# Performance work log

Hardware: AMD Instinct MI355X
Metric: run time of the kernel (lower is better)

The kernel has to match this reference:

```python
import jax, jax.numpy as jnp
import numpy as np
import math

D_MODEL = 1024
N_HEADS = 16
HEAD_DIM = D_MODEL // N_HEADS
B, T = 4, 2048


def setup_inputs() -> dict:
    key = jax.random.key(0)
    k1, k2, k3, k4, k5 = jax.random.split(key, 5)
    s = 1.0 / math.sqrt(D_MODEL)
    return {
        "x": jax.random.normal(k1, (B, T, D_MODEL), dtype=jnp.float32),
        "qkv_w": jax.random.normal(k2, (3 * D_MODEL, D_MODEL), dtype=jnp.float32) * s,
        "qkv_b": jax.random.normal(k3, (3 * D_MODEL,), dtype=jnp.float32) * 0.02,
        "out_w": jax.random.normal(k4, (D_MODEL, D_MODEL), dtype=jnp.float32) * s,
        "out_b": jax.random.normal(k5, (D_MODEL,), dtype=jnp.float32) * 0.02,
    }


def reference(x, qkv_w, qkv_b, out_w, out_b) -> jnp.ndarray:
    b, t, c = x.shape
    h, hd = N_HEADS, HEAD_DIM
    # qkv projection: [B,T,3C]
    qkv = jnp.einsum("btc,oc->bto", x, qkv_w) + qkv_b
    qkv = qkv.reshape(b, t, 3, h, hd).transpose(2, 0, 3, 1, 4)  # [3,B,H,T,hd]
    q, k, v = qkv[0], qkv[1], qkv[2]
    scale = 1.0 / math.sqrt(hd)
    attn = jnp.einsum("bhqd,bhkd->bhqk", q, k) * scale  # [B,H,T,T]
    causal = jnp.triu(jnp.ones((t, t), dtype=bool), k=1)
    attn = jnp.where(causal, -jnp.inf, attn)
    attn = jax.nn.softmax(attn, axis=-1)
    out = jnp.einsum("bhqk,bhkd->bhqd", attn, v)  # [B,H,T,hd]
    out = out.transpose(0, 2, 1, 3).reshape(b, t, c)
    return jnp.einsum("btc,oc->bto", out, out_w) + out_b
```

## Files before the change

kernel.cpp:

```cpp
#include <hip/hip_runtime.h>
#include <stdint.h>
#include <stddef.h>

#define TT 2048
#define NH 16
#define HD 64
#define CM 1024
#define QSCALE 0.1803368801f
#define PPAD 72

typedef float f32x4  __attribute__((ext_vector_type(4)));
typedef short bf16x8 __attribute__((ext_vector_type(8)));

static __device__ __forceinline__ unsigned short f32_to_bf16(float f) {
    union { float f; unsigned u; } c; c.f = f;
    unsigned u = c.u;
    u += 0x7FFFu + ((u >> 16) & 1u);
    return (unsigned short)(u >> 16);
}

static __device__ __forceinline__ unsigned pack_bf16_trunc(float lo, float hi) {
    return __builtin_amdgcn_perm(__float_as_uint(hi), __float_as_uint(lo), 0x07060302u);
}

static __device__ __forceinline__ void glds16(const unsigned short* g, unsigned short* l) {
    __builtin_amdgcn_global_load_lds(
        (const __attribute__((address_space(1))) unsigned int*)g,
        (__attribute__((address_space(3))) unsigned int*)l,
        16, 0, 0);
}

static __device__ __forceinline__ void hard_barrier() {
    asm volatile("s_waitcnt vmcnt(0) lgkmcnt(0)" ::: "memory");
    __syncthreads();
}

__global__ __launch_bounds__(256) void cast_all(
    const float* __restrict__ x, const float* __restrict__ w1,
    const float* __restrict__ w2,
    unsigned short* __restrict__ X16, unsigned short* __restrict__ W1o,
    unsigned short* __restrict__ W2o) {
    int i = blockIdx.x * blockDim.x + threadIdx.x;
    const float* src; unsigned short* dst; int j;
    if (i < 2097152)      { src = x;  dst = X16; j = i; }
    else if (i < 2883584) { src = w1; dst = W1o; j = i - 2097152; }
    else                  { src = w2; dst = W2o; j = i - 2883584; }
    float4 v = ((const float4*)src)[j];
    ushort4 o;
    o.x = f32_to_bf16(v.x); o.y = f32_to_bf16(v.y);
    o.z = f32_to_bf16(v.z); o.w = f32_to_bf16(v.w);
    ((ushort4*)dst)[j] = o;
}

template<bool SWAP>
__device__ __forceinline__ void gemm_core_dbuf(
    const unsigned short* __restrict__ A,
    const unsigned short* __restrict__ Bm,
    int K, int m0, int n0,
    unsigned short* lds,
    f32x4 acc[4][4])
{
    const int tid  = threadIdx.x;
    const int lane = tid & 63;
    const int wm   = ((tid >> 6) >> 1) * 64;
    const int wn   = ((tid >> 6) & 1) * 64;
    const int l15  = lane & 15;
    const int quad = lane >> 4;

    unsigned short* ldsA = lds;
    unsigned short* ldsB = lds + 8192;

    const int c1 = tid, c2 = tid + 256;
    const unsigned short* gA1 = A  + (size_t)(m0 + (c1 >> 2)) * K + (c1 & 3) * 8;
    const unsigned short* gA2 = A  + (size_t)(m0 + (c2 >> 2)) * K + (c2 & 3) * 8;
    const unsigned short* gB1 = Bm + (size_t)(n0 + (c1 >> 2)) * K + (c1 & 3) * 8;
    const unsigned short* gB2 = Bm + (size_t)(n0 + (c2 >> 2)) * K + (c2 & 3) * 8;
    unsigned short* dA1 = ldsA + (c1 & ~63) * 8;
    unsigned short* dA2 = ldsA + (c2 & ~63) * 8;
    unsigned short* dB1 = ldsB + (c1 & ~63) * 8;
    unsigned short* dB2 = ldsB + (c2 & ~63) * 8;

    glds16(gA1, dA1); glds16(gA2, dA2);
    glds16(gB1, dB1); glds16(gB2, dB2);
    gA1 += 32; gA2 += 32; gB1 += 32; gB2 += 32;

    int step = 0;
    for (int k0 = 0; k0 < K; k0 += 32, step ^= 1) {
        hard_barrier();
        if (k0 + 32 < K) {
            const int nx = (step ^ 1) * 4096;
            glds16(gA1, dA1 + nx); glds16(gA2, dA2 + nx);
            glds16(gB1, dB1 + nx); glds16(gB2, dB2 + nx);
            gA1 += 32; gA2 += 32; gB1 += 32; gB2 += 32;
        }
        const unsigned short* tA = ldsA + step * 4096;
        const unsigned short* tB = ldsB + step * 4096;

        bf16x8 af[4], bfr[4];
        #pragma unroll
        for (int mi = 0; mi < 4; ++mi)
            af[mi] = *(const bf16x8*)(tA + (wm + mi * 16 + l15) * 32 + quad * 8);
        #pragma unroll
        for (int ni = 0; ni < 4; ++ni)
            bfr[ni] = *(const bf16x8*)(tB + (wn + ni * 16 + l15) * 32 + quad * 8);

        #pragma unroll
        for (int mi = 0; mi < 4; ++mi)
            #pragma unroll
            for (int ni = 0; ni < 4; ++ni)
                acc[mi][ni] = SWAP
                    ? __builtin_amdgcn_mfma_f32_16x16x32_bf16(bfr[ni], af[mi], acc[mi][ni], 0, 0, 0)
                    : __builtin_amdgcn_mfma_f32_16x16x32_bf16(af[mi], bfr[ni], acc[mi][ni], 0, 0, 0);
    }
}

__global__ __launch_bounds__(256, 2) void gemm_qkv(
    const unsigned short* __restrict__ X,
    const unsigned short* __restrict__ W,
    const float* __restrict__ bias,
    unsigned short* __restrict__ Qb,
    unsigned short* __restrict__ Kb,
    unsigned short* __restrict__ Vt)
{
    __shared__ __align__(16) unsigned short lds[16384];
    const int m0 = blockIdx.y * 128;
    const int n0 = blockIdx.x * 128;

    f32x4 acc[4][4];
    f32x4 z = {0.f, 0.f, 0.f, 0.f};
    #pragma unroll
    for (int mi = 0; mi < 4; ++mi)
        #pragma unroll
        for (int ni = 0; ni < 4; ++ni) acc[mi][ni] = z;

    const bool qk = (n0 < 2048);
    if (qk) gemm_core_dbuf<true >(X, W, CM, m0, n0, lds, acc);
    else    gemm_core_dbuf<false>(X, W, CM, m0, n0, lds, acc);

    const int tid  = threadIdx.x;
    const int lane = tid & 63;
    const int w    = tid >> 6;
    const int wm   = (w >> 1) * 64;
    const int wn   = (w & 1) * 64;
    const int l15  = lane & 15;
    const int quad = lane >> 4;
    const int b_idx = m0 >> 11;
    const int t0 = m0 & 2047;

    if (!qk) {
        hard_barrier();
        #pragma unroll
        for (int half = 0; half < 2; ++half) {
            if ((w & 1) == half) {
                #pragma unroll
                for (int ni = 0; ni < 4; ++ni) {
                    const int orow = ni * 16 + l15;
                    const float bv = bias[n0 + half * 64 + orow];
                    #pragma unroll
                    for (int mi = 0; mi < 4; ++mi) {
                        uint2 pk;
                        pk.x = (unsigned)f32_to_bf16(acc[mi][ni][0] + bv) |
                               ((unsigned)f32_to_bf16(acc[mi][ni][1] + bv) << 16);
                        pk.y = (unsigned)f32_to_bf16(acc[mi][ni][2] + bv) |
                               ((unsigned)f32_to_bf16(acc[mi][ni][3] + bv) << 16);
                        *(uint2*)(lds + orow * 136 + wm + mi * 16 + quad * 4) = pk;
                    }
                }
            }
            hard_barrier();
            {
                const int row = tid >> 2, seg = tid & 3;
                const int o   = n0 + half * 64 + row;
                const int oin = o & 1023;
                const int hh  = oin >> 6, d = oin & 63;
                unsigned short* dst = Vt + ((size_t)((b_idx << 4) + hh) * HD + d) * TT
                                        + t0 + seg * 32;
                const unsigned short* src = lds + row * 136 + seg * 32;
                #pragma unroll
                for (int u = 0; u < 4; ++u)
                    *(uint4*)(dst + u * 8) = *(const uint4*)(src + u * 8);
            }
            hard_barrier();
        }
        return;
    }

    const int region = n0 >> 10;
    unsigned short* dst0 = region ? Kb : Qb;
    const float scl = region ? 1.0f : QSCALE;
    #pragma unroll
    for (int mi = 0; mi < 4; ++mi) {
        const int gm = m0 + wm + mi * 16 + l15;
        const int b  = gm >> 11, t = gm & 2047;
        #pragma unroll
        for (int ni = 0; ni < 4; ++ni) {
            const int o  = n0 + wn + ni * 16 + quad * 4;
            const float4 bv = *(const float4*)(bias + o);
            const int oin = o & 1023;
            const int hh = oin >> 6, d = oin & 63;
            const int bh = (b << 4) + hh;
            const float v0 = (acc[mi][ni][0] + bv.x) * scl;
            const float v1 = (acc[mi][ni][1] + bv.y) * scl;
            const float v2 = (acc[mi][ni][2] + bv.z) * scl;
            const float v3 = (acc[mi][ni][3] + bv.w) * scl;
            uint2 pk;
            pk.x = (unsigned)f32_to_bf16(v0) | ((unsigned)f32_to_bf16(v1) << 16);
            pk.y = (unsigned)f32_to_bf16(v2) | ((unsigned)f32_to_bf16(v3) << 16);
            *(uint2*)(dst0 + (((size_t)(bh * TT + t)) << 6) + d) = pk;
        }
    }
}

__global__ __launch_bounds__(256, 2) void attn_kernel(
    const unsigned short* __restrict__ Qb,
    const unsigned short* __restrict__ Kb,
    const unsigned short* __restrict__ Vt,
    unsigned short* __restrict__ CTX)
{
    __shared__ __align__(16) unsigned short Kl[2][64 * 64];
    __shared__ __align__(16) unsigned short Vl[2][64 * 64];
    __shared__ __align__(16) unsigned short Pl[8][16 * PPAD];

    const int pair = blockIdx.x;
    const int h = blockIdx.y, b = blockIdx.z;
    const int tid  = threadIdx.x;
    const int lane = tid & 63;
    const int w    = tid >> 6;
    const int l15  = lane & 15;
    const int quad = lane >> 4;
    const int sw   = l15 & 7;
    const int bh   = b * NH + h;

    const unsigned short* Kbase = Kb + (size_t)bh * TT * HD;
    const unsigned short* Vbase = Vt + (size_t)bh * HD * TT;
    const f32x4 z = {0.f, 0.f, 0.f, 0.f};

    const int c1 = tid, c2 = tid + 256;
    const int row1 = c1 >> 3, col1 = ((c1 & 7) ^ (row1 & 7)) * 8;
    const int row2 = c2 >> 3, col2 = ((c2 & 7) ^ (row2 & 7)) * 8;
    unsigned short* dK1 = &Kl[0][(c1 & ~63) * 8];
    unsigned short* dK2 = &Kl[0][(c2 & ~63) * 8];
    unsigned short* dV1 = &Vl[0][(c1 & ~63) * 8];
    unsigned short* dV2 = &Vl[0][(c2 & ~63) * 8];

    for (int j = 0; j < 2; ++j) {
        const int qt = j ? pair : 15 - pair;
        const int kt_last = 2 * qt + 1;
        const int qb0 = qt * 128;

        const unsigned short* kp1 = Kbase + (size_t)row1 * HD + col1;
        const unsigned short* kp2 = Kbase + (size_t)row2 * HD + col2;
        const unsigned short* vp1 = Vbase + (size_t)row1 * TT + col1;
        const unsigned short* vp2 = Vbase + (size_t)row2 * TT + col2;

        bf16x8 qf[2][2];
        #pragma unroll
        for (int f = 0; f < 2; ++f) {
            const unsigned short* qr =
                Qb + (size_t)(bh * TT + qb0 + f * 64 + w * 16 + l15) * HD + quad * 8;
            qf[f][0] = *(const bf16x8*)(qr);
            qf[f][1] = *(const bf16x8*)(qr + 32);
        }

        f32x4 o_acc[2][4];
        #pragma unroll
        for (int f = 0; f < 2; ++f)
            #pragma unroll
            for (int di = 0; di < 4; ++di) o_acc[f][di] = z;
        float lrun[2] = {0.f, 0.f};

        hard_barrier();
        glds16(kp1, dK1); glds16(kp2, dK2);
        glds16(vp1, dV1); glds16(vp2, dV2);
        kp1 += 64 * HD; kp2 += 64 * HD; vp1 += 64; vp2 += 64;

        for (int kt = 0; kt <= kt_last; ++kt) {
            const int cur = kt & 1;
            hard_barrier();
            if (kt < kt_last) {
                const int nx = (cur ^ 1) * 4096;
                glds16(kp1, dK1 + nx); glds16(kp2, dK2 + nx);
                glds16(vp1, dV1 + nx); glds16(vp2, dV2 + nx);
                kp1 += 64 * HD; kp2 += 64 * HD; vp1 += 64; vp2 += 64;
            }

            const unsigned short* Kt = Kl[cur];
            const unsigned short* Vtile = Vl[cur];
            const bool f0act = (kt < kt_last);

            f32x4 s0[4], s1[4];
            #pragma unroll
            for (int ni = 0; ni < 4; ++ni) {
                const unsigned short* kr = Kt + (ni * 16 + l15) * 64;
                bf16x8 kf0 = *(const bf16x8*)(kr + ((quad ^ sw) * 8));
                bf16x8 kf1 = *(const bf16x8*)(kr + (((quad + 4) ^ sw) * 8));
                if (f0act) {
                    f32x4 a = __builtin_amdgcn_mfma_f32_16x16x32_bf16(kf0, qf[0][0], z, 0, 0, 0);
                    s0[ni] = __builtin_amdgcn_mfma_f32_16x16x32_bf16(kf1, qf[0][1], a, 0, 0, 0);
                }
                f32x4 a1 = __builtin_amdgcn_mfma_f32_16x16x32_bf16(kf0, qf[1][0], z, 0, 0, 0);
                s1[ni] = __builtin_amdgcn_mfma_f32_16x16x32_bf16(kf1, qf[1][1], a1, 0, 0, 0);
            }

            const int qloc = w * 16 + l15;
            if (f0act && kt == 2 * qt) {
                #pragma unroll
                for (int ni = 0; ni < 4; ++ni)
                    #pragma unroll
                    for (int r = 0; r < 4; ++r)
                        if (ni * 16 + quad * 4 + r > qloc) s0[ni][r] = -1e30f;
            }
            if (kt == kt_last) {
                #pragma unroll
                for (int ni = 0; ni < 4; ++ni)
                    #pragma unroll
                    for (int r = 0; r < 4; ++r)
                        if (ni * 16 + quad * 4 + r > qloc) s1[ni][r] = -1e30f;
            }

            #define SOFTMAX_P(S, F)                                              \
            {                                                                    \
                float acc_l = 0.f;                                               \
                _Pragma("unroll")                                                \
                for (int ni = 0; ni < 4; ++ni)                                   \
                    _Pragma("unroll")                                            \
                    for (int r = 0; r < 4; ++r) {                                \
                        float p = __builtin_amdgcn_exp2f(S[ni][r]);              \
                        S[ni][r] = p;                                            \
                        acc_l += p;                                              \
                    }                                                            \
                lrun[F] += acc_l;                                                \
                unsigned short* pwf = Pl[w * 2 + F];                             \
                _Pragma("unroll")                                                \
                for (int ni = 0; ni < 4; ++ni) {                                 \
                    uint2 pk;                                                    \
                    pk.x = pack_bf16_trunc(S[ni][0], S[ni][1]);                  \
                    pk.y = pack_bf16_trunc(S[ni][2], S[ni][3]);                  \
                    *(uint2*)(pwf + l15 * PPAD + ni * 16 + quad * 4) = pk;       \
                }                                                                \
            }

            if (f0act) SOFTMAX_P(s0, 0);
            SOFTMAX_P(s1, 1);
            #undef SOFTMAX_P

            asm volatile("s_waitcnt lgkmcnt(0)" ::: "memory");

            const unsigned short* pw0 = Pl[w * 2 + 0];
            const unsigned short* pw1 = Pl[w * 2 + 1];
            if (f0act) {
                #pragma unroll
                for (int c = 0; c < 2; ++c) {
                    bf16x8 pf0 = *(const bf16x8*)(pw0 + l15 * PPAD + c * 32 + quad * 8);
                    bf16x8 pf1 = *(const bf16x8*)(pw1 + l15 * PPAD + c * 32 + quad * 8);
                    #pragma unroll
                    for (int di = 0; di < 4; ++di) {
                        const unsigned short* vr = Vtile + (di * 16 + l15) * 64
                                                 + (((c * 4 + quad) ^ sw) * 8);
                        bf16x8 vf = *(const bf16x8*)(vr);
                        o_acc[0][di] = __builtin_amdgcn_mfma_f32_16x16x32_bf16(vf, pf0, o_acc[0][di], 0, 0, 0);
                        o_acc[1][di] = __builtin_amdgcn_mfma_f32_16x16x32_bf16(vf, pf1, o_acc[1][di], 0, 0, 0);
                    }
                }
            } else {
                #pragma unroll
                for (int c = 0; c < 2; ++c) {
                    bf16x8 pf1 = *(const bf16x8*)(pw1 + l15 * PPAD + c * 32 + quad * 8);
                    #pragma unroll
                    for (int di = 0; di < 4; ++di) {
                        const unsigned short* vr = Vtile + (di * 16 + l15) * 64
                                                 + (((c * 4 + quad) ^ sw) * 8);
                        bf16x8 vf = *(const bf16x8*)(vr);
                        o_acc[1][di] = __builtin_amdgcn_mfma_f32_16x16x32_bf16(vf, pf1, o_acc[1][di], 0, 0, 0);
                    }
                }
            }
        }

        #pragma unroll
        for (int f = 0; f < 2; ++f) {
            float lt = lrun[f];
            lt += __shfl_xor(lt, 16);
            lt += __shfl_xor(lt, 32);
            const float inv = 1.0f / lt;
            unsigned short* crow =
                CTX + (size_t)(b * TT + qb0 + f * 64 + w * 16 + l15) * CM + h * HD;
            #pragma unroll
            for (int di = 0; di < 4; ++di) {
                uint2 pk;
                pk.x = (unsigned)f32_to_bf16(o_acc[f][di][0] * inv) |
                       ((unsigned)f32_to_bf16(o_acc[f][di][1] * inv) << 16);
                pk.y = (unsigned)f32_to_bf16(o_acc[f][di][2] * inv) |
                       ((unsigned)f32_to_bf16(o_acc[f][di][3] * inv) << 16);
                *(uint2*)(crow + di * 16 + quad * 4) = pk;
            }
        }
    }
}

__global__ __launch_bounds__(256, 2) void gemm_out(
    const unsigned short* __restrict__ CTX,
    const unsigned short* __restrict__ W,
    const float* __restrict__ bias,
    float* __restrict__ out)
{
    __shared__ __align__(16) unsigned short lds[16384];
    const int m0 = blockIdx.y * 128;
    const int n0 = blockIdx.x * 128;

    f32x4 acc[4][4];
    f32x4 z = {0.f, 0.f, 0.f, 0.f};
    #pragma unroll
    for (int mi = 0; mi < 4; ++mi)
        #pragma unroll
        for (int ni = 0; ni < 4; ++ni) acc[mi][ni] = z;

    gemm_core_dbuf<true>(CTX, W, CM, m0, n0, lds, acc);

    const int tid  = threadIdx.x;
    const int lane = tid & 63;
    const int w    = tid >> 6;
    const int wm   = (w >> 1) * 64;
    const int wn   = (w & 1) * 64;
    const int l15  = lane & 15;
    const int quad = lane >> 4;

    #pragma unroll
    for (int mi = 0; mi < 4; ++mi) {
        const int gm = m0 + wm + mi * 16 + l15;
        float* orow = out + (size_t)gm * CM;
        #pragma unroll
        for (int ni = 0; ni < 4; ++ni) {
            const int o = n0 + wn + ni * 16 + quad * 4;
            const float4 bv = *(const float4*)(bias + o);
            float4 v;
            v.x = acc[mi][ni][0] + bv.x;
            v.y = acc[mi][ni][1] + bv.y;
            v.z = acc[mi][ni][2] + bv.z;
            v.w = acc[mi][ni][3] + bv.w;
            *(float4*)(orow + o) = v;
        }
    }
}

extern "C" void kernel_launch(void* const* d_in, const int* in_sizes, int n_in,
                              void* d_out, int out_size, void* d_ws, size_t ws_size,
                              hipStream_t stream) {
    const float* x     = (const float*)d_in[0];
    const float* qkv_w = (const float*)d_in[1];
    const float* qkv_b = (const float*)d_in[2];
    const float* out_w = (const float*)d_in[3];
    const float* out_b = (const float*)d_in[4];
    float* out = (float*)d_out;

    char* ws = (char*)d_ws;
    unsigned short* X16 = (unsigned short*)(ws + 0);
    unsigned short* W1  = (unsigned short*)(ws + 16777216);
    unsigned short* W2  = (unsigned short*)(ws + 23068672);
    unsigned short* Qb  = (unsigned short*)(ws + 25165824);
    unsigned short* Kb  = (unsigned short*)(ws + 41943040);
    unsigned short* Vt  = (unsigned short*)(ws + 58720256);
    unsigned short* CTX = (unsigned short*)(ws + 75497472);

    cast_all<<<12288, 256, 0, stream>>>(x, qkv_w, out_w, X16, W1, W2);

    gemm_qkv<<<dim3(24, 64), 256, 0, stream>>>(X16, W1, qkv_b, Qb, Kb, Vt);
    attn_kernel<<<dim3(8, NH, 4), 256, 0, stream>>>(Qb, Kb, Vt, CTX);
    gemm_out<<<dim3(8, 64), 256, 0, stream>>>(CTX, W2, out_b, out);
}
```

Baseline: 262.5 us.

## Swizzle GEMM LDS layout and split attention into one q-tile per block

New measurement: 255.4 us. 1.03x faster.

```diff
diff --git a/kernel.cpp b/kernel.cpp
--- a/kernel.cpp
+++ b/kernel.cpp
@@ -66,15 +66,18 @@
     const int wn   = ((tid >> 6) & 1) * 64;
     const int l15  = lane & 15;
     const int quad = lane >> 4;
+    const int rsw  = l15 & 3;
 
     unsigned short* ldsA = lds;
     unsigned short* ldsB = lds + 8192;
 
     const int c1 = tid, c2 = tid + 256;
-    const unsigned short* gA1 = A  + (size_t)(m0 + (c1 >> 2)) * K + (c1 & 3) * 8;
-    const unsigned short* gA2 = A  + (size_t)(m0 + (c2 >> 2)) * K + (c2 & 3) * 8;
-    const unsigned short* gB1 = Bm + (size_t)(n0 + (c1 >> 2)) * K + (c1 & 3) * 8;
-    const unsigned short* gB2 = Bm + (size_t)(n0 + (c2 >> 2)) * K + (c2 & 3) * 8;
+    const int r1 = c1 >> 2, s1 = ((c1 & 3) ^ (r1 & 3)) * 8;
+    const int r2 = c2 >> 2, s2 = ((c2 & 3) ^ (r2 & 3)) * 8;
+    const unsigned short* gA1 = A  + (size_t)(m0 + r1) * K + s1;
+    const unsigned short* gA2 = A  + (size_t)(m0 + r2) * K + s2;
+    const unsigned short* gB1 = Bm + (size_t)(n0 + r1) * K + s1;
+    const unsigned short* gB2 = Bm + (size_t)(n0 + r2) * K + s2;
     unsigned short* dA1 = ldsA + (c1 & ~63) * 8;
     unsigned short* dA2 = ldsA + (c2 & ~63) * 8;
     unsigned short* dB1 = ldsB + (c1 & ~63) * 8;
@@ -95,14 +98,15 @@
         }
         const unsigned short* tA = ldsA + step * 4096;
         const unsigned short* tB = ldsB + step * 4096;
+        const int ro = (quad ^ rsw) * 8;
 
         bf16x8 af[4], bfr[4];
         #pragma unroll
         for (int mi = 0; mi < 4; ++mi)
-            af[mi] = *(const bf16x8*)(tA + (wm + mi * 16 + l15) * 32 + quad * 8);
+            af[mi] = *(const bf16x8*)(tA + (wm + mi * 16 + l15) * 32 + ro);
         #pragma unroll
         for (int ni = 0; ni < 4; ++ni)
-            bfr[ni] = *(const bf16x8*)(tB + (wn + ni * 16 + l15) * 32 + quad * 8);
+            bfr[ni] = *(const bf16x8*)(tB + (wn + ni * 16 + l15) * 32 + ro);
 
         #pragma unroll
         for (int mi = 0; mi < 4; ++mi)
@@ -221,18 +225,20 @@
     __shared__ __align__(16) unsigned short Vl[2][64 * 64];
     __shared__ __align__(16) unsigned short Pl[8][16 * PPAD];
 
-    const int pair = blockIdx.x;
-    const int h = blockIdx.y, b = blockIdx.z;
+    const int id = blockIdx.x;
+    const int qt = 15 - (id >> 6);
+    const int bh = id & 63;
+    const int b  = bh >> 4, h = bh & 15;
     const int tid  = threadIdx.x;
     const int lane = tid & 63;
     const int w    = tid >> 6;
     const int l15  = lane & 15;
     const int quad = lane >> 4;
     const int sw   = l15 & 7;
-    const int bh   = b * NH + h;
-
-    const unsigned short* Kbase = Kb + (size_t)bh * TT * HD;
-    const unsigned short* Vbase = Vt + (size_t)bh * HD * TT;
+    const int bhh  = b * NH + h;
+
+    const unsigned short* Kbase = Kb + (size_t)bhh * TT * HD;
+    const unsigned short* Vbase = Vt + (size_t)bhh * HD * TT;
     const f32x4 z = {0.f, 0.f, 0.f, 0.f};
 
     const int c1 = tid, c2 = tid + 256;
@@ -243,157 +249,153 @@
     unsigned short* dV1 = &Vl[0][(c1 & ~63) * 8];
     unsigned short* dV2 = &Vl[0][(c2 & ~63) * 8];
 
-    for (int j = 0; j < 2; ++j) {
-        const int qt = j ? pair : 15 - pair;
-        const int kt_last = 2 * qt + 1;
-        const int qb0 = qt * 128;
-
-        const unsigned short* kp1 = Kbase + (size_t)row1 * HD + col1;
-        const unsigned short* kp2 = Kbase + (size_t)row2 * HD + col2;
-        const unsigned short* vp1 = Vbase + (size_t)row1 * TT + col1;
-        const unsigned short* vp2 = Vbase + (size_t)row2 * TT + col2;
-
-        bf16x8 qf[2][2];
-        #pragma unroll
-        for (int f = 0; f < 2; ++f) {
-            const unsigned short* qr =
-                Qb + (size_t)(bh * TT + qb0 + f * 64 + w * 16 + l15) * HD + quad * 8;
-            qf[f][0] = *(const bf16x8*)(qr);
-            qf[f][1] = *(const bf16x8*)(qr + 32);
-        }
-
-        f32x4 o_acc[2][4];
-        #pragma unroll
-        for (int f = 0; f < 2; ++f)
+    const int kt_last = 2 * qt + 1;
+    const int qb0 = qt * 128;
+
+    const unsigned short* kp1 = Kbase + (size_t)row1 * HD + col1;
+    const unsigned short* kp2 = Kbase + (size_t)row2 * HD + col2;
+    const unsigned short* vp1 = Vbase + (size_t)row1 * TT + col1;
+    const unsigned short* vp2 = Vbase + (size_t)row2 * TT + col2;
+
+    bf16x8 qf[2][2];
+    #pragma unroll
+    for (int f = 0; f < 2; ++f) {
+        const unsigned short* qr =
+            Qb + (size_t)(bhh * TT + qb0 + f * 64 + w * 16 + l15) * HD + quad * 8;
+        qf[f][0] = *(const bf16x8*)(qr);
+        qf[f][1] = *(const bf16x8*)(qr + 32);
+    }
+
+    f32x4 o_acc[2][4];
+    #pragma unroll
+    for (int f = 0; f < 2; ++f)
+        #pragma unroll
+        for (int di = 0; di < 4; ++di) o_acc[f][di] = z;
+    float lrun[2] = {0.f, 0.f};
+
+    glds16(kp1, dK1); glds16(kp2, dK2);
+    glds16(vp1, dV1); glds16(vp2, dV2);
+    kp1 += 64 * HD; kp2 += 64 * HD; vp1 += 64; vp2 += 64;
+
+    for (int kt = 0; kt <= kt_last; ++kt) {
+        const int cur = kt & 1;
+        hard_barrier();
+        if (kt < kt_last) {
+            const int nx = (cur ^ 1) * 4096;
+            glds16(kp1, dK1 + nx); glds16(kp2, dK2 + nx);
+            glds16(vp1, dV1 + nx); glds16(vp2, dV2 + nx);
+            kp1 += 64 * HD; kp2 += 64 * HD; vp1 += 64; vp2 += 64;
+        }
+
+        const unsigned short* Kt = Kl[cur];
+        const unsigned short* Vtile = Vl[cur];
+        const bool f0act = (kt < kt_last);
+
+        f32x4 s0[4], s1[4];
+        #pragma unroll
+        for (int ni = 0; ni < 4; ++ni) {
+            const unsigned short* kr = Kt + (ni * 16 + l15) * 64;
+            bf16x8 kf0 = *(const bf16x8*)(kr + ((quad ^ sw) * 8));
+            bf16x8 kf1 = *(const bf16x8*)(kr + (((quad + 4) ^ sw) * 8));
+            if (f0act) {
+                f32x4 a = __builtin_amdgcn_mfma_f32_16x16x32_bf16(kf0, qf[0][0], z, 0, 0, 0);
+                s0[ni] = __builtin_amdgcn_mfma_f32_16x16x32_bf16(kf1, qf[0][1], a, 0, 0, 0);
+            }
+            f32x4 a1 = __builtin_amdgcn_mfma_f32_16x16x32_bf16(kf0, qf[1][0], z, 0, 0, 0);
+            s1[ni] = __builtin_amdgcn_mfma_f32_16x16x32_bf16(kf1, qf[1][1], a1, 0, 0, 0);
+        }
+
+        const int qloc = w * 16 + l15;
+        if (f0act && kt == 2 * qt) {
             #pragma unroll
-            for (int di = 0; di < 4; ++di) o_acc[f][di] = z;
-        float lrun[2] = {0.f, 0.f};
-
-        hard_barrier();
-        glds16(kp1, dK1); glds16(kp2, dK2);
-        glds16(vp1, dV1); glds16(vp2, dV2);
-        kp1 += 64 * HD; kp2 += 64 * HD; vp1 += 64; vp2 += 64;
-
-        for (int kt = 0; kt <= kt_last; ++kt) {
-            const int cur = kt & 1;
-            hard_barrier();
-            if (kt < kt_last) {
-                const int nx = (cur ^ 1) * 4096;
-                glds16(kp1, dK1 + nx); glds16(kp2, dK2 + nx);
-                glds16(vp1, dV1 + nx); glds16(vp2, dV2 + nx);
-                kp1 += 64 * HD; kp2 += 64 * HD; vp1 += 64; vp2 += 64;
-            }
-
-            const unsigned short* Kt = Kl[cur];
-            const unsigned short* Vtile = Vl[cur];
-            const bool f0act = (kt < kt_last);
-
-            f32x4 s0[4], s1[4];
+            for (int ni = 0; ni < 4; ++ni)
+                #pragma unroll
+                for (int r = 0; r < 4; ++r)
+                    if (ni * 16 + quad * 4 + r > qloc) s0[ni][r] = -1e30f;
+        }
+        if (kt == kt_last) {
             #pragma unroll
-            for (int ni = 0; ni < 4; ++ni) {
-                const unsigned short* kr = Kt + (ni * 16 + l15) * 64;
-                bf16x8 kf0 = *(const bf16x8*)(kr + ((quad ^ sw) * 8));
-                bf16x8 kf1 = *(const bf16x8*)(kr + (((quad + 4) ^ sw) * 8));
-                if (f0act) {
-                    f32x4 a = __builtin_amdgcn_mfma_f32_16x16x32_bf16(kf0, qf[0][0], z, 0, 0, 0);
-                    s0[ni] = __builtin_amdgcn_mfma_f32_16x16x32_bf16(kf1, qf[0][1], a, 0, 0, 0);
-                }
-                f32x4 a1 = __builtin_amdgcn_mfma_f32_16x16x32_bf16(kf0, qf[1][0], z, 0, 0, 0);
-                s1[ni] = __builtin_amdgcn_mfma_f32_16x16x32_bf16(kf1, qf[1][1], a1, 0, 0, 0);
-            }
-
-            const int qloc = w * 16 + l15;
-            if (f0act && kt == 2 * qt) {
-                #pragma unroll
-                for (int ni = 0; ni < 4; ++ni)
-                    #pragma unroll
-                    for (int r = 0; r < 4; ++r)
-                        if (ni * 16 + quad * 4 + r > qloc) s0[ni][r] = -1e30f;
-            }
-            if (kt == kt_last) {
-                #pragma unroll
-                for (int ni = 0; ni < 4; ++ni)
-                    #pragma unroll
-                    for (int r = 0; r < 4; ++r)
-                        if (ni * 16 + quad * 4 + r > qloc) s1[ni][r] = -1e30f;
-            }
-
-            #define SOFTMAX_P(S, F)                                              \
-            {                                                                    \
-                float acc_l = 0.f;                                               \
-                _Pragma("unroll")                                                \
-                for (int ni = 0; ni < 4; ++ni)                                   \
-                    _Pragma("unroll")                                            \
-                    for (int r = 0; r < 4; ++r) {                                \
-                        float p = __builtin_amdgcn_exp2f(S[ni][r]);              \
-                        S[ni][r] = p;                                            \
-                        acc_l += p;                                              \
-                    }                                                            \
-                lrun[F] += acc_l;                                                \
-                unsigned short* pwf = Pl[w * 2 + F];                             \
-                _Pragma("unroll")                                                \
-                for (int ni = 0; ni < 4; ++ni) {                                 \
-                    uint2 pk;                                                    \
-                    pk.x = pack_bf16_trunc(S[ni][0], S[ni][1]);                  \
-                    pk.y = pack_bf16_trunc(S[ni][2], S[ni][3]);                  \
-                    *(uint2*)(pwf + l15 * PPAD + ni * 16 + quad * 4) = pk;       \
-                }                                                                \
-            }
-
-            if (f0act) SOFTMAX_P(s0, 0);
-            SOFTMAX_P(s1, 1);
-            #undef SOFTMAX_P
-
-            asm volatile("s_waitcnt lgkmcnt(0)" ::: "memory");
-
-            const unsigned short* pw0 = Pl[w * 2 + 0];
-            const unsigned short* pw1 = Pl[w * 2 + 1];
-            if (f0act) {
-                #pragma unroll
-                for (int c = 0; c < 2; ++c) {
-                    bf16x8 pf0 = *(const bf16x8*)(pw0 + l15 * PPAD + c * 32 + quad * 8);
-                    bf16x8 pf1 = *(const bf16x8*)(pw1 + l15 * PPAD + c * 32 + quad * 8);
-                    #pragma unroll
-                    for (int di = 0; di < 4; ++di) {
-                        const unsigned short* vr = Vtile + (di * 16 + l15) * 64
-                                                 + (((c * 4 + quad) ^ sw) * 8);
-                        bf16x8 vf = *(const bf16x8*)(vr);
-                        o_acc[0][di] = __builtin_amdgcn_mfma_f32_16x16x32_bf16(vf, pf0, o_acc[0][di], 0, 0, 0);
-                        o_acc[1][di] = __builtin_amdgcn_mfma_f32_16x16x32_bf16(vf, pf1, o_acc[1][di], 0, 0, 0);
-                    }
-                }
-            } else {
-                #pragma unroll
-                for (int c = 0; c < 2; ++c) {
-                    bf16x8 pf1 = *(const bf16x8*)(pw1 + l15 * PPAD + c * 32 + quad * 8);
-                    #pragma unroll
-                    for (int di = 0; di < 4; ++di) {
-                        const unsigned short* vr = Vtile + (di * 16 + l15) * 64
-                                                 + (((c * 4 + quad) ^ sw) * 8);
-                        bf16x8 vf = *(const bf16x8*)(vr);
-                        o_acc[1][di] = __builtin_amdgcn_mfma_f32_16x16x32_bf16(vf, pf1, o_acc[1][di], 0, 0, 0);
-                    }
+            for (int ni = 0; ni < 4; ++ni)
+                #pragma unroll
+                for (int r = 0; r < 4; ++r)
+                    if (ni * 16 + quad * 4 + r > qloc) s1[ni][r] = -1e30f;
+        }
+
+        #define SOFTMAX_P(S, F)                                              \
+        {                                                                    \
+            float acc_l = 0.f;                                               \
+            _Pragma("unroll")                                                \
+            for (int ni = 0; ni < 4; ++ni)                                   \
+                _Pragma("unroll")                                            \
+                for (int r = 0; r < 4; ++r) {                                \
+                    float p = __builtin_amdgcn_exp2f(S[ni][r]);              \
+                    S[ni][r] = p;                                            \
+                    acc_l += p;                                              \
+                }                                                            \
+            lrun[F] += acc_l;                                                \
+            unsigned short* pwf = Pl[w * 2 + F];                             \
+            _Pragma("unroll")                                                \
+            for (int ni = 0; ni < 4; ++ni) {                                 \
+                uint2 pk;                                                    \
+                pk.x = pack_bf16_trunc(S[ni][0], S[ni][1]);                  \
+                pk.y = pack_bf16_trunc(S[ni][2], S[ni][3]);                  \
+                *(uint2*)(pwf + l15 * PPAD + ni * 16 + quad * 4) = pk;       \
+            }                                                                \
+        }
+
+        if (f0act) SOFTMAX_P(s0, 0);
+        SOFTMAX_P(s1, 1);
+        #undef SOFTMAX_P
+
+        asm volatile("s_waitcnt lgkmcnt(0)" ::: "memory");
+
+        const unsigned short* pw0 = Pl[w * 2 + 0];
+        const unsigned short* pw1 = Pl[w * 2 + 1];
+        if (f0act) {
+            #pragma unroll
+            for (int c = 0; c < 2; ++c) {
+                bf16x8 pf0 = *(const bf16x8*)(pw0 + l15 * PPAD + c * 32 + quad * 8);
+                bf16x8 pf1 = *(const bf16x8*)(pw1 + l15 * PPAD + c * 32 + quad * 8);
+                #pragma unroll
+                for (int di = 0; di < 4; ++di) {
+                    const unsigned short* vr = Vtile + (di * 16 + l15) * 64
+                                             + (((c * 4 + quad) ^ sw) * 8);
+                    bf16x8 vf = *(const bf16x8*)(vr);
+                    o_acc[0][di] = __builtin_amdgcn_mfma_f32_16x16x32_bf16(vf, pf0, o_acc[0][di], 0, 0, 0);
+                    o_acc[1][di] = __builtin_amdgcn_mfma_f32_16x16x32_bf16(vf, pf1, o_acc[1][di], 0, 0, 0);
                 }
             }
-        }
-
-        #pragma unroll
-        for (int f = 0; f < 2; ++f) {
-            float lt = lrun[f];
-            lt += __shfl_xor(lt, 16);
-            lt += __shfl_xor(lt, 32);
-            const float inv = 1.0f / lt;
-            unsigned short* crow =
-                CTX + (size_t)(b * TT + qb0 + f * 64 + w * 16 + l15) * CM + h * HD;
+        } else {
             #pragma unroll
-            for (int di = 0; di < 4; ++di) {
-                uint2 pk;
-                pk.x = (unsigned)f32_to_bf16(o_acc[f][di][0] * inv) |
-                       ((unsigned)f32_to_bf16(o_acc[f][di][1] * inv) << 16);
-                pk.y = (unsigned)f32_to_bf16(o_acc[f][di][2] * inv) |
-                       ((unsigned)f32_to_bf16(o_acc[f][di][3] * inv) << 16);
-                *(uint2*)(crow + di * 16 + quad * 4) = pk;
+            for (int c = 0; c < 2; ++c) {
+                bf16x8 pf1 = *(const bf16x8*)(pw1 + l15 * PPAD + c * 32 + quad * 8);
+                #pragma unroll
+                for (int di = 0; di < 4; ++di) {
+                    const unsigned short* vr = Vtile + (di * 16 + l15) * 64
+                                             + (((c * 4 + quad) ^ sw) * 8);
+                    bf16x8 vf = *(const bf16x8*)(vr);
+                    o_acc[1][di] = __builtin_amdgcn_mfma_f32_16x16x32_bf16(vf, pf1, o_acc[1][di], 0, 0, 0);
+                }
             }
+        }
+    }
+
+    #pragma unroll
+    for (int f = 0; f < 2; ++f) {
+        float lt = lrun[f];
+        lt += __shfl_xor(lt, 16);
+        lt += __shfl_xor(lt, 32);
+        const float inv = 1.0f / lt;
+        unsigned short* crow =
+            CTX + (size_t)(b * TT + qb0 + f * 64 + w * 16 + l15) * CM + h * HD;
+        #pragma unroll
+        for (int di = 0; di < 4; ++di) {
+            uint2 pk;
+            pk.x = (unsigned)f32_to_bf16(o_acc[f][di][0] * inv) |
+                   ((unsigned)f32_to_bf16(o_acc[f][di][1] * inv) << 16);
+            pk.y = (unsigned)f32_to_bf16(o_acc[f][di][2] * inv) |
+                   ((unsigned)f32_to_bf16(o_acc[f][di][3] * inv) << 16);
+            *(uint2*)(crow + di * 16 + quad * 4) = pk;
         }
     }
 }
@@ -465,6 +467,6 @@
     cast_all<<<12288, 256, 0, stream>>>(x, qkv_w, out_w, X16, W1, W2);
 
     gemm_qkv<<<dim3(24, 64), 256, 0, stream>>>(X16, W1, qkv_b, Qb, Kb, Vt);
-    attn_kernel<<<dim3(8, NH, 4), 256, 0, stream>>>(Qb, Kb, Vt, CTX);
+    attn_kernel<<<1024, 256, 0, stream>>>(Qb, Kb, Vt, CTX);
     gemm_out<<<dim3(8, 64), 256, 0, stream>>>(CTX, W2, out_b, out);
 }
```
